# Kernel tuning notes

Measured on AMD Instinct MI355X. Metric: run time of the kernel, lower is better.

Reference implementation:

```python
import jax, jax.numpy as jnp
import numpy as np

NUM_GRAPHS = 64

def _mlp(x, Wa, ba, Wb, bb):
    # 2-layer MLP: Linear -> ReLU -> Linear
    return jnp.maximum(x @ Wa + ba, 0.0) @ Wb + bb

def setup_inputs() -> dict:
    key = jax.random.key(0)
    ks = jax.random.split(key, 16)
    N1, E1, N2, E2 = 20000, 640000, 640000, 1280000
    d_x1, d_x2, d_e2, d_h, d_et, d_out = 32, 32, 16, 64, 32, 32
    inp = {
        'x1': jax.random.normal(ks[0], (N1, d_x1), jnp.float32),
        'x2': jax.random.normal(ks[1], (N2, d_x2), jnp.float32),
        'edge_index1': jax.random.randint(ks[2], (2, E1), 0, N1),
        'edge_index2': jax.random.randint(ks[3], (2, E2), 0, N2),
        'x1_batch': jnp.sort(jax.random.randint(ks[4], (N1,), 0, NUM_GRAPHS)),
        'edge_attr2': jax.random.normal(ks[5], (E2, d_e2), jnp.float32),
        # mlp2 (DGCN edge network): in = d_x2 + d_e2 = 48 -> 64 -> 32
        'W2a': jax.random.normal(ks[6], (d_x2 + d_e2, d_h), jnp.float32) * 0.05,
        'b2a': jnp.zeros((d_h,), jnp.float32),
        'W2b': jax.random.normal(ks[7], (d_h, d_et), jnp.float32) * 0.05,
        'b2b': jnp.zeros((d_et,), jnp.float32),
        # mlp (MOLGCN edge-conditioned network): in = d_x1 + d_et = 64 -> 64 -> 32
        'W1a': jax.random.normal(ks[8], (d_x1 + d_et, d_h), jnp.float32) * 0.05,
        'b1a': jnp.zeros((d_h,), jnp.float32),
        'W1b': jax.random.normal(ks[9], (d_h, d_out), jnp.float32) * 0.05,
        'b1b': jnp.zeros((d_out,), jnp.float32),
    }
    return inp

def reference(x1, x2, edge_index1, edge_index2, x1_batch, edge_attr2,
              W2a, b2a, W2b, b2b, W1a, b1a, W1b, b1b):
    N1, N2 = x1.shape[0], x2.shape[0]
    # --- DGCN over graph 2: message = mlp2([x_src, edge_attr]), sum-aggregate at dst ---
    s2, d2 = edge_index2[0], edge_index2[1]
    msg2 = _mlp(jnp.concatenate([x2[s2], edge_attr2], axis=-1), W2a, b2a, W2b, b2b)  # [E2, d_et]
    e_t = jax.ops.segment_sum(msg2, d2, num_segments=N2)  # [N2, d_et]; N2 == E1 (line graph)
    # --- MOLGCN over graph 1: edge-conditioned message = mlp([x_src, e_t]), sum at dst ---
    s1, d1 = edge_index1[0], edge_index1[1]
    msg1 = _mlp(jnp.concatenate([x1[s1], e_t], axis=-1), W1a, b1a, W1b, b1b)  # [E1, d_out]
    h = jax.ops.segment_sum(msg1, d1, num_segments=N1)  # [N1, d_out]
    # --- global add pool over graphs, then squeeze()/2 ---
    pooled = jax.ops.segment_sum(h, x1_batch, num_segments=NUM_GRAPHS)  # [G, d_out]
    return jnp.squeeze(pooled) / 2.0
```

## Files before the change

kernel.cpp:

```cpp
#include <hip/hip_runtime.h>
#include <hip/hip_bf16.h>


#define NUM_GRAPHS 64
#define CAP 4608
#define CURSTRIDE 16
#define EPB 8192
#define NCVT 2048

typedef __attribute__((ext_vector_type(8))) short bf16x8;
typedef __attribute__((ext_vector_type(4))) float f32x4;

__device__ __forceinline__ unsigned short f2bf(float x) {
    __hip_bfloat16 b = __float2bfloat16(x);
    return *(unsigned short*)&b;
}
__device__ __forceinline__ float bf2f(unsigned int u16) {
    unsigned short us = (unsigned short)u16;
    __hip_bfloat16 b = *(__hip_bfloat16*)&us;
    return __bfloat162float(b);
}
__device__ __forceinline__ unsigned int pack2(float lo, float hi) {
    return (unsigned int)f2bf(lo) | ((unsigned int)f2bf(hi) << 16);
}
__device__ __forceinline__ uint4 cvt8(const float* src) {
    const float4* s4 = (const float4*)src;
    float4 a = s4[0], b = s4[1];
    return make_uint4(pack2(a.x, a.y), pack2(a.z, a.w),
                      pack2(b.x, b.y), pack2(b.z, b.w));
}
__device__ __forceinline__ int swz(int row, int kb) {
    return row * 128 + (kb ^ ((row & 7) << 4));
}


__global__ __launch_bounds__(256) void k_prep0(
    const float* __restrict__ W2a, const float* __restrict__ b2a,
    const float* __restrict__ W2b, const float* __restrict__ b2b,
    const float* __restrict__ W1a, const float* __restrict__ b1a,
    const float* __restrict__ W1b, const float* __restrict__ b1b,
    unsigned char* __restrict__ wpack, int* __restrict__ cur, int ncur)
{
    const int tid = threadIdx.x;
    if (blockIdx.x == 0) {
        unsigned char* img1 = wpack;
        unsigned char* img2 = wpack + 12672;
        for (int i = tid; i < 64 * 64; i += 256) {
            int n = i >> 6, k = i & 63;
            float v1 = (k < 48) ? W2a[k * 64 + n] : 0.0f;
            *(unsigned short*)(img1 + n * 128 + ((2 * k) ^ ((n & 7) << 4))) = f2bf(v1);
            *(unsigned short*)(img2 + n * 128 + ((2 * k) ^ ((n & 7) << 4))) = f2bf(W1a[k * 64 + n]);
        }
        for (int i = tid; i < 32 * 64; i += 256) {
            int n = i >> 6, k = i & 63;
            *(unsigned short*)(img1 + 8192 + n * 128 + ((2 * k) ^ ((n & 7) << 4))) = f2bf(W2b[k * 32 + n]);
            *(unsigned short*)(img2 + 8192 + n * 128 + ((2 * k) ^ ((n & 7) << 4))) = f2bf(W1b[k * 32 + n]);
        }
        if (tid < 64) {
            ((float*)(img1 + 12288))[tid] = b2a[tid];
            ((float*)(img2 + 12288))[tid] = b1a[tid];
        }
        if (tid < 32) {
            ((float*)(img1 + 12544))[tid] = b2b[tid];
            ((float*)(img2 + 12544))[tid] = b1b[tid];
        }
    } else {
        for (int i = tid; i < ncur; i += 256) cur[i] = 0;
    }
}


__global__ __launch_bounds__(256) void k_bscat_cvt(
    const int* __restrict__ ei2, int E2, const int* __restrict__ ei1, int E1,
    int* __restrict__ cur, uint2* __restrict__ mid, int NB2, int NBT, int Etot, int NBB,
    const float* __restrict__ x2, uint4* __restrict__ x2b,
    const float* __restrict__ x1, uint4* __restrict__ x1b,
    const float* __restrict__ ea2, uint4* __restrict__ ea2b,
    long xn2, long xn1, long xne)
{
    __shared__ unsigned int buck[EPB];
    __shared__ int hist[512];
    __shared__ int gbase[512];
    __shared__ int wloc[512];

    const int tid = threadIdx.x;
    if (blockIdx.x >= NBB) {
        const long tot = xn2 + xn1 + xne;
        const long stride = (long)NCVT * 256;
        for (long i = (long)(blockIdx.x - NBB) * 256 + tid; i < tot; i += stride) {
            if (i < xn2) x2b[i] = cvt8(x2 + i * 8);
            else if (i < xn2 + xn1) { long j = i - xn2; x1b[j] = cvt8(x1 + j * 8); }
            else { long j = i - xn2 - xn1; ea2b[j] = cvt8(ea2 + j * 8); }
        }
        return;
    }

    const long start = (long)blockIdx.x * EPB;
    const int nloc = (int)(((long)Etot - start) < EPB ? ((long)Etot - start) : EPB);
    if (nloc <= 0) return;

    for (int i = tid; i < NBT; i += 256) hist[i] = 0;
    __syncthreads();

    for (int k = tid; k < nloc; k += 256) {
        const long i = start + k;
        int b, dlo;
        if (i < E2) {
            int d = ei2[E2 + i]; b = d >> 11; dlo = d & 2047;
        } else {
            int j = (int)(i - E2);
            int d = ei1[E1 + j]; b = NB2 + (d >> 7); dlo = d & 127;
        }
        buck[k] = (unsigned)b | ((unsigned)dlo << 16);
        atomicAdd(&hist[b], 1);
    }
    __syncthreads();

    for (int i = tid; i < NBT; i += 256) {
        const int c = hist[i];
        gbase[i] = (c > 0) ? atomicAdd(&cur[i * CURSTRIDE], c) : 0;
        wloc[i] = 0;
    }
    __syncthreads();

    for (int k = tid; k < nloc; k += 256) {
        const long i = start + k;
        const unsigned bv = buck[k];
        const int b = (int)(bv & 0xffffu), dlo = (int)(bv >> 16);
        int e, s;
        if (i < E2) { e = (int)i; s = ei2[i]; }
        else        { int j = (int)(i - E2); e = j; s = ei1[j]; }
        const int pos = gbase[b] + atomicAdd(&wloc[b], 1);
        if (pos < CAP)
            mid[(size_t)b * CAP + pos] =
                make_uint2((unsigned)e | ((unsigned)dlo << 21), (unsigned)s);
    }
}


__global__ __launch_bounds__(256) void k_csr(
    const int* __restrict__ cur, const uint2* __restrict__ mid,
    uint2* __restrict__ ord, int NB2, int E2)
{
    __shared__ int cnt[2048];
    __shared__ int cnt2[2048];
    __shared__ int red[256];
    __shared__ int wpart[4];
    __shared__ int sCarry;

    const int b = blockIdx.x, tid = threadIdx.x;
    const bool g2 = (b < NB2);
    const int span = g2 ? 2048 : 128;
    const int lo = g2 ? 0 : NB2;
    const int fill = min(cur[b * CURSTRIDE], CAP);

    int part = 0;
    for (int k = lo + tid; k < b; k += 256) part += min(cur[k * CURSTRIDE], CAP);
    red[tid] = part;
    __syncthreads();
    for (int off = 128; off >= 1; off >>= 1) {
        if (tid < off) red[tid] += red[tid + off];
        __syncthreads();
    }
    const int outBase = (g2 ? 0 : E2) + red[0];

    for (int k = tid; k < span; k += 256) cnt[k] = 0;
    __syncthreads();

    const size_t mbase = (size_t)b * CAP;
    for (int i = tid; i < fill; i += 256)
        atomicAdd(&cnt[mid[mbase + i].x >> 21], 1);
    __syncthreads();

    if (tid == 0) sCarry = 0;
    __syncthreads();
    const int lane = tid & 63, wv = tid >> 6;
    for (int c0 = 0; c0 < span; c0 += 256) {
        const int idx = c0 + tid;
        int v = (idx < span) ? cnt[idx] : 0;
        int inc = v;
        #pragma unroll
        for (int off = 1; off < 64; off <<= 1) {
            int nv = __shfl_up(inc, off, 64);
            if (lane >= off) inc += nv;
        }
        if (lane == 63) wpart[wv] = inc;
        __syncthreads();
        int wpre = 0;
        for (int wq = 0; wq < wv; ++wq) wpre += wpart[wq];
        const int excl = sCarry + wpre + inc - v;
        const int tot = wpart[0] + wpart[1] + wpart[2] + wpart[3];
        __syncthreads();
        if (idx < span) cnt[idx] = excl;
        if (tid == 0) sCarry += tot;
        __syncthreads();
    }

    for (int k = tid; k < span; k += 256) cnt2[k] = 0;
    __syncthreads();

    for (int i = tid; i < fill; i += 256) {
        uint2 r = mid[mbase + i];
        const int dl = (int)(r.x >> 21);
        const int rk = atomicAdd(&cnt2[dl], 1);
        ord[outBase + cnt[dl] + rk] = make_uint2(r.x, r.y | ((unsigned)b << 20));
    }
}


__global__ __launch_bounds__(256) void k_msg2_agg(
    const float* __restrict__ x2f, const uint4* __restrict__ x2b,
    const float* __restrict__ ea2, const uint4* __restrict__ ea2b,
    const uint2* __restrict__ ord, const unsigned char* __restrict__ wimg,
    unsigned int* __restrict__ e_t, int E, int use_bf16, int use_ea2b)
{
    __shared__ __align__(16) unsigned char sBuf[32768];
    unsigned short* smsg = (unsigned short*)sBuf;
    int* sdst = (int*)(sBuf + 16896);
    int* rstart = (int*)(sBuf + 16896 + 1032);
    unsigned long long* wmaskS = (unsigned long long*)(sBuf + 16896 + 1032 + 1032);

    const int tid = threadIdx.x;
    const int base = blockIdx.x * 256, p = base + tid;

    int e = 0, s = 0, d = -1, dp_ = -1, dn_ = -1;
    if (p < E) {
        uint2 o = ord[p];
        e = (int)(o.x & 0x1FFFFFu); s = (int)(o.y & 0xFFFFFu);
        d = ((int)(o.y >> 20) << 11) + (int)(o.x >> 21);
    }
    if (tid == 0) {
        if (base > 0) { uint2 o = ord[base - 1]; dp_ = ((int)(o.y >> 20) << 11) + (int)(o.x >> 21); }
        if (base + 256 < E) { uint2 o = ord[base + 256]; dn_ = ((int)(o.y >> 20) << 11) + (int)(o.x >> 21); }
    }

    {
        uint4 ch[8];
        if (use_bf16) {
            const uint4* xr = x2b + (size_t)s * 4;
            #pragma unroll
            for (int c = 0; c < 4; ++c) ch[c] = xr[c];
        } else {
            const float4* xs = (const float4*)(x2f + (size_t)s * 32);
            #pragma unroll
            for (int c = 0; c < 4; ++c) {
                float4 a = xs[2 * c], b = xs[2 * c + 1];
                ch[c].x = pack2(a.x, a.y); ch[c].y = pack2(a.z, a.w);
                ch[c].z = pack2(b.x, b.y); ch[c].w = pack2(b.z, b.w);
            }
        }
        if (use_ea2b) {
            ch[4] = ea2b[(size_t)e * 2];
            ch[5] = ea2b[(size_t)e * 2 + 1];
        } else {
            const float4* es = (const float4*)(ea2 + (size_t)e * 16);
            #pragma unroll
            for (int c = 0; c < 2; ++c) {
                float4 a = es[2 * c], b = es[2 * c + 1];
                ch[4 + c].x = pack2(a.x, a.y); ch[4 + c].y = pack2(a.z, a.w);
                ch[4 + c].z = pack2(b.x, b.y); ch[4 + c].w = pack2(b.z, b.w);
            }
        }
        ch[6] = make_uint4(0, 0, 0, 0);
        ch[7] = make_uint4(0, 0, 0, 0);
        #pragma unroll
        for (int c = 0; c < 8; ++c)
            *(uint4*)(sBuf + swz(tid, c * 16)) = ch[c];
    }
    __syncthreads();

    const int lane = tid & 63, wv = tid >> 6;
    const int lr = lane & 15, lk = lane >> 4;
    const int band = wv * 64;
    const unsigned char* gWa = wimg;
    const unsigned char* gWb = wimg + 8192;
    const float* gba = (const float*)(wimg + 12288);
    const float* gbb = (const float*)(wimg + 12544);

    f32x4 accA[4][4];
    #pragma unroll
    for (int n = 0; n < 4; ++n) {
        float bv = gba[n * 16 + lr];
        #pragma unroll
        for (int m = 0; m < 4; ++m) accA[m][n] = (f32x4){bv, bv, bv, bv};
    }
    #pragma unroll
    for (int ks = 0; ks < 2; ++ks) {
        const int kb = ks * 64 + lk * 16;
        bf16x8 af[4], bfr[4];
        #pragma unroll
        for (int m = 0; m < 4; ++m)
            af[m] = *(const bf16x8*)(sBuf + swz(band + m * 16 + lr, kb));
        #pragma unroll
        for (int n = 0; n < 4; ++n) {
            int rw = n * 16 + lr;
            bfr[n] = *(const bf16x8*)(gWa + rw * 128 + (kb ^ ((rw & 7) << 4)));
        }
        #pragma unroll
        for (int m = 0; m < 4; ++m)
            #pragma unroll
            for (int n = 0; n < 4; ++n)
                accA[m][n] = __builtin_amdgcn_mfma_f32_16x16x32_bf16(af[m], bfr[n], accA[m][n], 0, 0, 0);
    }
    #pragma unroll
    for (int m = 0; m < 4; ++m)
        #pragma unroll
        for (int n = 0; n < 4; ++n)
            #pragma unroll
            for (int rr = 0; rr < 4; ++rr) {
                int grow = band + m * 16 + lk * 4 + rr;
                int cb = 2 * (n * 16 + lr);
                *(unsigned short*)(sBuf + swz(grow, cb)) = f2bf(fmaxf(accA[m][n][rr], 0.0f));
            }

    f32x4 accB[4][2];
    #pragma unroll
    for (int n = 0; n < 2; ++n) {
        float bv = gbb[n * 16 + lr];
        #pragma unroll
        for (int m = 0; m < 4; ++m) accB[m][n] = (f32x4){bv, bv, bv, bv};
    }
    #pragma unroll
    for (int ks = 0; ks < 2; ++ks) {
        const int kb = ks * 64 + lk * 16;
        bf16x8 af[4], bfr[2];
        #pragma unroll
        for (int m = 0; m < 4; ++m)
            af[m] = *(const bf16x8*)(sBuf + swz(band + m * 16 + lr, kb));
        #pragma unroll
        for (int n = 0; n < 2; ++n) {
            int rw = n * 16 + lr;
            bfr[n] = *(const bf16x8*)(gWb + rw * 128 + (kb ^ ((rw & 7) << 4)));
        }
        #pragma unroll
        for (int m = 0; m < 4; ++m)
            #pragma unroll
            for (int n = 0; n < 2; ++n)
                accB[m][n] = __builtin_amdgcn_mfma_f32_16x16x32_bf16(af[m], bfr[n], accB[m][n], 0, 0, 0);
    }
    __syncthreads();

    #pragma unroll
    for (int m = 0; m < 4; ++m)
        #pragma unroll
        for (int n = 0; n < 2; ++n)
            #pragma unroll
            for (int rr = 0; rr < 4; ++rr)
                smsg[(band + m * 16 + lk * 4 + rr) * 33 + n * 16 + lr] = f2bf(accB[m][n][rr]);
    sdst[tid] = d;
    if (tid == 0) { sdst[256] = dn_; sdst[257] = dp_; }
    __syncthreads();

    const bool leader = (p < E) && (tid == 0 || sdst[tid - 1] != d);
    wmaskS[wv] = __ballot(leader);
    __syncthreads();

    int nruns = __popcll(wmaskS[0]) + __popcll(wmaskS[1]) + __popcll(wmaskS[2]) + __popcll(wmaskS[3]);
    if (leader) {
        int before = __popcll(wmaskS[wv] & ((1ULL << lane) - 1));
        for (int w = 0; w < wv; ++w) before += __popcll(wmaskS[w]);
        rstart[before] = tid;
    }
    const int vcnt = (E - base < 256) ? (E - base) : 256;
    if (tid == 0) rstart[nruns] = vcnt;
    __syncthreads();

    const int sPrev = sdst[257];
    const int ntask = nruns * 32;
    for (int task = tid; task < ntask; task += 256) {
        const int run = task >> 5, c = task & 31;
        const int rs = rstart[run], re = rstart[run + 1];
        const int dd = sdst[rs];
        float acc = 0.0f;
        for (int qq = rs; qq < re; ++qq) acc += bf2f(smsg[qq * 33 + c]);
        const bool gs = (rs > 0) || (base == 0) || (sPrev != dd);
        const bool ge = (re < 256) || (sdst[256] != dd);
        if (gs && ge) {
            ((unsigned short*)e_t)[(size_t)dd * 32 + c] = f2bf(acc);
        } else {
            unsigned int* a32 = e_t + (size_t)dd * 16 + (c >> 1);
            const int sh = (c & 1) * 16;
            unsigned int old = *a32;
            while (true) {
                float cur2 = bf2f((old >> sh) & 0xffffu);
                unsigned int nb = f2bf(cur2 + acc);
                unsigned int nv = (old & ~(0xffffu << sh)) | (nb << sh);
                unsigned int prev = atomicCAS(a32, old, nv);
                if (prev == old) break;
                old = prev;
            }
        }
    }
}


__global__ __launch_bounds__(256) void k_msg1_agg(
    const float* __restrict__ x1f, const uint4* __restrict__ x1b,
    const unsigned int* __restrict__ e_t,
    const uint2* __restrict__ ord, const unsigned char* __restrict__ wimg,
    float* __restrict__ h, int E, int NB2, int use_bf16)
{
    __shared__ __align__(16) unsigned char sBuf[32768];
    unsigned short* smsg = (unsigned short*)sBuf;
    int* sdst = (int*)(sBuf + 16896);
    int* rstart = (int*)(sBuf + 16896 + 1032);
    unsigned long long* wmaskS = (unsigned long long*)(sBuf + 16896 + 1032 + 1032);

    const int tid = threadIdx.x;
    const int base = blockIdx.x * 256, p = base + tid;

    int e = 0, s = 0, d = -1, dp_ = -1, dn_ = -1;
    if (p < E) {
        uint2 o = ord[p];
        e = (int)(o.x & 0x1FFFFFu); s = (int)(o.y & 0xFFFFFu);
        d = (((int)(o.y >> 20) - NB2) << 7) + (int)(o.x >> 21);
    }
    if (tid == 0) {
        if (base > 0) { uint2 o = ord[base - 1]; dp_ = (((int)(o.y >> 20) - NB2) << 7) + (int)(o.x >> 21); }
        if (base + 256 < E) { uint2 o = ord[base + 256]; dn_ = (((int)(o.y >> 20) - NB2) << 7) + (int)(o.x >> 21); }
    }

    {
        uint4 ch[8];
        if (use_bf16) {
            const uint4* xr = x1b + (size_t)s * 4;
            #pragma unroll
            for (int c = 0; c < 4; ++c) ch[c] = xr[c];
        } else {
            const float4* xs = (const float4*)(x1f + (size_t)s * 32);
            #pragma unroll
            for (int c = 0; c < 4; ++c) {
                float4 a = xs[2 * c], b = xs[2 * c + 1];
                ch[c].x = pack2(a.x, a.y); ch[c].y = pack2(a.z, a.w);
                ch[c].z = pack2(b.x, b.y); ch[c].w = pack2(b.z, b.w);
            }
        }
        const uint4* er = (const uint4*)(e_t + (size_t)e * 16);
        #pragma unroll
        for (int c = 0; c < 4; ++c) ch[4 + c] = er[c];
        #pragma unroll
        for (int c = 0; c < 8; ++c)
            *(uint4*)(sBuf + swz(tid, c * 16)) = ch[c];
    }
    __syncthreads();

    const int lane = tid & 63, wv = tid >> 6;
    const int lr = lane & 15, lk = lane >> 4;
    const int band = wv * 64;
    const unsigned char* gWa = wimg;
    const unsigned char* gWb = wimg + 8192;
    const float* gba = (const float*)(wimg + 12288);
    const float* gbb = (const float*)(wimg + 12544);

    f32x4 accA[4][4];
    #pragma unroll
    for (int n = 0; n < 4; ++n) {
        float bv = gba[n * 16 + lr];
        #pragma unroll
        for (int m = 0; m < 4; ++m) accA[m][n] = (f32x4){bv, bv, bv, bv};
    }
    #pragma unroll
    for (int ks = 0; ks < 2; ++ks) {
        const int kb = ks * 64 + lk * 16;
        bf16x8 af[4], bfr[4];
        #pragma unroll
        for (int m = 0; m < 4; ++m)
            af[m] = *(const bf16x8*)(sBuf + swz(band + m * 16 + lr, kb));
        #pragma unroll
        for (int n = 0; n < 4; ++n) {
            int rw = n * 16 + lr;
            bfr[n] = *(const bf16x8*)(gWa + rw * 128 + (kb ^ ((rw & 7) << 4)));
        }
        #pragma unroll
        for (int m = 0; m < 4; ++m)
            #pragma unroll
            for (int n = 0; n < 4; ++n)
                accA[m][n] = __builtin_amdgcn_mfma_f32_16x16x32_bf16(af[m], bfr[n], accA[m][n], 0, 0, 0);
    }
    #pragma unroll
    for (int m = 0; m < 4; ++m)
        #pragma unroll
        for (int n = 0; n < 4; ++n)
            #pragma unroll
            for (int rr = 0; rr < 4; ++rr) {
                int grow = band + m * 16 + lk * 4 + rr;
                int cb = 2 * (n * 16 + lr);
                *(unsigned short*)(sBuf + swz(grow, cb)) = f2bf(fmaxf(accA[m][n][rr], 0.0f));
            }

    f32x4 accB[4][2];
    #pragma unroll
    for (int n = 0; n < 2; ++n) {
        float bv = gbb[n * 16 + lr];
        #pragma unroll
        for (int m = 0; m < 4; ++m) accB[m][n] = (f32x4){bv, bv, bv, bv};
    }
    #pragma unroll
    for (int ks = 0; ks < 2; ++ks) {
        const int kb = ks * 64 + lk * 16;
        bf16x8 af[4], bfr[2];
        #pragma unroll
        for (int m = 0; m < 4; ++m)
            af[m] = *(const bf16x8*)(sBuf + swz(band + m * 16 + lr, kb));
        #pragma unroll
        for (int n = 0; n < 2; ++n) {
            int rw = n * 16 + lr;
            bfr[n] = *(const bf16x8*)(gWb + rw * 128 + (kb ^ ((rw & 7) << 4)));
        }
        #pragma unroll
        for (int m = 0; m < 4; ++m)
            #pragma unroll
            for (int n = 0; n < 2; ++n)
                accB[m][n] = __builtin_amdgcn_mfma_f32_16x16x32_bf16(af[m], bfr[n], accB[m][n], 0, 0, 0);
    }
    __syncthreads();

    #pragma unroll
    for (int m = 0; m < 4; ++m)
        #pragma unroll
        for (int n = 0; n < 2; ++n)
            #pragma unroll
            for (int rr = 0; rr < 4; ++rr)
                smsg[(band + m * 16 + lk * 4 + rr) * 33 + n * 16 + lr] = f2bf(accB[m][n][rr]);
    sdst[tid] = d;
    if (tid == 0) { sdst[256] = dn_; sdst[257] = dp_; }
    __syncthreads();

    const bool leader = (p < E) && (tid == 0 || sdst[tid - 1] != d);
    wmaskS[wv] = __ballot(leader);
    __syncthreads();

    int nruns = __popcll(wmaskS[0]) + __popcll(wmaskS[1]) + __popcll(wmaskS[2]) + __popcll(wmaskS[3]);
    if (leader) {
        int before = __popcll(wmaskS[wv] & ((1ULL << lane) - 1));
        for (int w = 0; w < wv; ++w) before += __popcll(wmaskS[w]);
        rstart[before] = tid;
    }
    const int vcnt = (E - base < 256) ? (E - base) : 256;
    if (tid == 0) rstart[nruns] = vcnt;
    __syncthreads();

    const int sPrev = sdst[257];
    const int ntask = nruns * 32;
    for (int task = tid; task < ntask; task += 256) {
        const int run = task >> 5, c = task & 31;
        const int rs = rstart[run], re = rstart[run + 1];
        const int dd = sdst[rs];
        float acc = 0.0f;
        for (int qq = rs; qq < re; ++qq) acc += bf2f(smsg[qq * 33 + c]);
        const bool gs = (rs > 0) || (base == 0) || (sPrev != dd);
        const bool ge = (re < 256) || (sdst[256] != dd);
        if (gs && ge) h[(size_t)dd * 32 + c] = acc;
        else atomicAdd(h + (size_t)dd * 32 + c, acc);
    }
}


__device__ __forceinline__ int lower_bound_i(const int* a, int n, int key) {
    int lo = 0, hi = n;
    while (lo < hi) {
        int mid = (lo + hi) >> 1;
        if (a[mid] < key) lo = mid + 1; else hi = mid;
    }
    return lo;
}

__global__ __launch_bounds__(256) void k_pool(const float* __restrict__ h,
                                              const int* __restrict__ batch,
                                              float* __restrict__ out, int N1) {
    const int g = blockIdx.x;
    const int lo = lower_bound_i(batch, N1, g);
    const int hi = lower_bound_i(batch, N1, g + 1);
    const int tid = threadIdx.x;
    const int c = tid & 31, rg = tid >> 5;
    float acc = 0.0f;
    for (int n = lo + rg; n < hi; n += 8) acc += h[(size_t)n * 32 + c];
    __shared__ float red[256];
    red[tid] = acc;
    __syncthreads();
    for (int off = 128; off >= 32; off >>= 1) {
        if (tid < off) red[tid] += red[tid + off];
        __syncthreads();
    }
    if (tid < 32) out[g * 32 + tid] = red[tid] * 0.5f;
}


extern "C" void kernel_launch(void* const* d_in, const int* in_sizes, int n_in,
                              void* d_out, int out_size, void* d_ws, size_t ws_size,
                              hipStream_t stream) {
    const float* x1  = (const float*)d_in[0];
    const float* x2  = (const float*)d_in[1];
    const int*   ei1 = (const int*)d_in[2];
    const int*   ei2 = (const int*)d_in[3];
    const int*   xb  = (const int*)d_in[4];
    const float* ea2 = (const float*)d_in[5];
    const float* W2a = (const float*)d_in[6];
    const float* b2a = (const float*)d_in[7];
    const float* W2b = (const float*)d_in[8];
    const float* b2b = (const float*)d_in[9];
    const float* W1a = (const float*)d_in[10];
    const float* b1a = (const float*)d_in[11];
    const float* W1b = (const float*)d_in[12];
    const float* b1b = (const float*)d_in[13];

    const int N1 = in_sizes[0] / 32;
    const int E1 = in_sizes[2] / 2;
    const int E2 = in_sizes[3] / 2;
    const int N2 = in_sizes[1] / 32;
    const int Etot = E2 + E1;

    const int NB2 = (N2 + 2047) >> 11;
    const int NB1 = (N1 + 127) >> 7;
    const int NBT = NB2 + NB1;

    const size_t sz_wpack = 25600;
    const size_t sz_cur   = (size_t)NBT * CURSTRIDE * 4;
    const size_t sz_et    = (size_t)N2 * 64;
    const size_t sz_h     = (size_t)N1 * 128;
    const size_t sz_ord   = (size_t)Etot * 8;
    const size_t sz_mid   = (size_t)NBT * CAP * 8;
    const size_t regA     = (sz_mid > sz_et + sz_h) ? sz_mid : (sz_et + sz_h);
    const size_t sz_x2b   = (size_t)N2 * 64;
    const size_t sz_x1b   = (size_t)N1 * 64;
    const size_t sz_ea2b  = (size_t)E2 * 32;
    const size_t need_x   = sz_ord + regA + sz_x2b + sz_x1b + sz_wpack + sz_cur;
    const size_t need_xe  = need_x + sz_ea2b;

    const int use_bf16 = (ws_size >= need_x) ? 1 : 0;
    const int use_ea2b = (ws_size >= need_xe) ? 1 : 0;

    char* w = (char*)d_ws;
    uint2* ord = (uint2*)w;            w += sz_ord;
    char* regionA = w;                 w += regA;
    uint4* x2b = (uint4*)w;            if (use_bf16) w += sz_x2b;
    uint4* x1b = (uint4*)w;            if (use_bf16) w += sz_x1b;
    uint4* ea2b = (uint4*)w;           if (use_ea2b) w += sz_ea2b;
    unsigned char* wpack = (unsigned char*)w;  w += sz_wpack;
    int* cur = (int*)w;

    unsigned int* e_t = (unsigned int*)regionA;
    float* h = (float*)(regionA + sz_et);
    uint2* mid = (uint2*)regionA;

    const int NBB = (Etot + EPB - 1) / EPB;
    const long xn2 = use_bf16 ? (long)N2 * 4 : 0;
    const long xn1 = use_bf16 ? (long)N1 * 4 : 0;
    const long xne = use_ea2b ? (long)E2 * 2 : 0;

    k_prep0<<<2, 256, 0, stream>>>(W2a, b2a, W2b, b2b, W1a, b1a, W1b, b1b,
                                   wpack, cur, NBT * CURSTRIDE);
    k_bscat_cvt<<<NBB + NCVT, 256, 0, stream>>>(
        ei2, E2, ei1, E1, cur, mid, NB2, NBT, Etot, NBB,
        x2, x2b, x1, x1b, ea2, ea2b, xn2, xn1, xne);
    k_csr<<<NBT, 256, 0, stream>>>(cur, mid, ord, NB2, E2);
    hipMemsetAsync(regionA, 0, sz_et + sz_h, stream);
    k_msg2_agg<<<(E2 + 255) / 256, 256, 0, stream>>>(
        x2, x2b, ea2, ea2b, ord, wpack, e_t, E2, use_bf16, use_ea2b);
    k_msg1_agg<<<(E1 + 255) / 256, 256, 0, stream>>>(
        x1, x1b, e_t, ord + E2, wpack + 12672, h, E1, NB2, use_bf16);
    k_pool<<<NUM_GRAPHS, 256, 0, stream>>>(h, xb, (float*)d_out, N1);
}
```

Baseline: 262.1 us.

## Store e_t rows in graph-1 CSR order so msg1 reads them contiguously

Splits the CSR build into two kernels. The graph-1 pass runs first and records the sorted rank of each line-graph node. The graph-2 pass then relabels its destinations with that rank, so msg2 aggregation writes e_t rows in the order msg1 consumes them. msg1 then reads e_t sequentially by its own position instead of gathering by edge id, which replaces a random 64-byte-row gather with coalesced loads. In exchange it adds an extra kernel launch, a rank array, and a random rank lookup in the graph-2 CSR pass, and graph-2 destinations may now be less clustered, which could hurt its segmented reduction.

```diff
diff --git a/kernel.cpp b/kernel.cpp
--- a/kernel.cpp
+++ b/kernel.cpp
@@ -138,40 +138,9 @@
 }
 
 
-__global__ __launch_bounds__(256) void k_csr(
-    const int* __restrict__ cur, const uint2* __restrict__ mid,
-    uint2* __restrict__ ord, int NB2, int E2)
-{
-    __shared__ int cnt[2048];
-    __shared__ int cnt2[2048];
-    __shared__ int red[256];
+__device__ __forceinline__ void lds_excl_scan(int* cnt, int span, int tid) {
     __shared__ int wpart[4];
     __shared__ int sCarry;
-
-    const int b = blockIdx.x, tid = threadIdx.x;
-    const bool g2 = (b < NB2);
-    const int span = g2 ? 2048 : 128;
-    const int lo = g2 ? 0 : NB2;
-    const int fill = min(cur[b * CURSTRIDE], CAP);
-
-    int part = 0;
-    for (int k = lo + tid; k < b; k += 256) part += min(cur[k * CURSTRIDE], CAP);
-    red[tid] = part;
-    __syncthreads();
-    for (int off = 128; off >= 1; off >>= 1) {
-        if (tid < off) red[tid] += red[tid + off];
-        __syncthreads();
-    }
-    const int outBase = (g2 ? 0 : E2) + red[0];
-
-    for (int k = tid; k < span; k += 256) cnt[k] = 0;
-    __syncthreads();
-
-    const size_t mbase = (size_t)b * CAP;
-    for (int i = tid; i < fill; i += 256)
-        atomicAdd(&cnt[mid[mbase + i].x >> 21], 1);
-    __syncthreads();
-
     if (tid == 0) sCarry = 0;
     __syncthreads();
     const int lane = tid & 63, wv = tid >> 6;
@@ -195,15 +164,90 @@
         if (tid == 0) sCarry += tot;
         __syncthreads();
     }
-
-    for (int k = tid; k < span; k += 256) cnt2[k] = 0;
-    __syncthreads();
-
+}
+
+
+__global__ __launch_bounds__(256) void k_csr1(
+    const int* __restrict__ cur, const uint2* __restrict__ mid,
+    uint2* __restrict__ ord1, int* __restrict__ rank1, int NB2)
+{
+    __shared__ int cnt[128];
+    __shared__ int cnt2[128];
+    __shared__ int red[256];
+
+    const int bl = blockIdx.x, tid = threadIdx.x;
+    const int bg = NB2 + bl;
+    const int fill = min(cur[bg * CURSTRIDE], CAP);
+
+    int part = 0;
+    for (int k = NB2 + tid; k < bg; k += 256) part += min(cur[k * CURSTRIDE], CAP);
+    red[tid] = part;
+    __syncthreads();
+    for (int off = 128; off >= 1; off >>= 1) {
+        if (tid < off) red[tid] += red[tid + off];
+        __syncthreads();
+    }
+    const int outBase = red[0];
+
+    if (tid < 128) { cnt[tid] = 0; cnt2[tid] = 0; }
+    __syncthreads();
+    const size_t mbase = (size_t)bg * CAP;
+    for (int i = tid; i < fill; i += 256)
+        atomicAdd(&cnt[mid[mbase + i].x >> 21], 1);
+    __syncthreads();
+    lds_excl_scan(cnt, 128, tid);
+    __syncthreads();
     for (int i = tid; i < fill; i += 256) {
         uint2 r = mid[mbase + i];
         const int dl = (int)(r.x >> 21);
         const int rk = atomicAdd(&cnt2[dl], 1);
-        ord[outBase + cnt[dl] + rk] = make_uint2(r.x, r.y | ((unsigned)b << 20));
+        const int o = outBase + cnt[dl] + rk;
+        ord1[o] = make_uint2(r.x, r.y | ((unsigned)bg << 20));
+        rank1[r.x & 0x1FFFFFu] = o;
+    }
+}
+
+
+__global__ __launch_bounds__(256) void k_csr2(
+    const int* __restrict__ cur, const uint2* __restrict__ mid,
+    uint2* __restrict__ ord2, const int* __restrict__ rank1, int E1)
+{
+    __shared__ int cnt[2048];
+    __shared__ int cnt2[2048];
+    __shared__ int red[256];
+
+    const int b = blockIdx.x, tid = threadIdx.x;
+    const int node0 = b << 11;
+    const int fill = min(cur[b * CURSTRIDE], CAP);
+
+    int part = 0;
+    for (int k = tid; k < b; k += 256) part += min(cur[k * CURSTRIDE], CAP);
+    red[tid] = part;
+    __syncthreads();
+    for (int off = 128; off >= 1; off >>= 1) {
+        if (tid < off) red[tid] += red[tid + off];
+        __syncthreads();
+    }
+    const int outBase = red[0];
+
+    for (int k = tid; k < 2048; k += 256) { cnt[k] = 0; cnt2[k] = 0; }
+    __syncthreads();
+    const size_t mbase = (size_t)b * CAP;
+    for (int i = tid; i < fill; i += 256)
+        atomicAdd(&cnt[mid[mbase + i].x >> 21], 1);
+    __syncthreads();
+    lds_excl_scan(cnt, 2048, tid);
+    __syncthreads();
+    for (int i = tid; i < fill; i += 256) {
+        uint2 r = mid[mbase + i];
+        const int dl = (int)(r.x >> 21);
+        const int e  = (int)(r.x & 0x1FFFFFu);
+        const int rk = atomicAdd(&cnt2[dl], 1);
+        const int o = outBase + cnt[dl] + rk;
+        unsigned key = (unsigned)rank1[node0 + dl];
+        if (key >= (unsigned)E1) key = 0;
+        ord2[o] = make_uint2((unsigned)e | ((key & 0x7FFu) << 21),
+                             r.y | ((key >> 11) << 20));
     }
 }
 
@@ -227,11 +271,11 @@
     if (p < E) {
         uint2 o = ord[p];
         e = (int)(o.x & 0x1FFFFFu); s = (int)(o.y & 0xFFFFFu);
-        d = ((int)(o.y >> 20) << 11) + (int)(o.x >> 21);
+        d = (int)((o.x >> 21) | ((o.y >> 20) << 11));
     }
     if (tid == 0) {
-        if (base > 0) { uint2 o = ord[base - 1]; dp_ = ((int)(o.y >> 20) << 11) + (int)(o.x >> 21); }
-        if (base + 256 < E) { uint2 o = ord[base + 256]; dn_ = ((int)(o.y >> 20) << 11) + (int)(o.x >> 21); }
+        if (base > 0) { uint2 o = ord[base - 1]; dp_ = (int)((o.x >> 21) | ((o.y >> 20) << 11)); }
+        if (base + 256 < E) { uint2 o = ord[base + 256]; dn_ = (int)((o.x >> 21) | ((o.y >> 20) << 11)); }
     }
 
     {
@@ -409,10 +453,10 @@
     const int tid = threadIdx.x;
     const int base = blockIdx.x * 256, p = base + tid;
 
-    int e = 0, s = 0, d = -1, dp_ = -1, dn_ = -1;
+    int s = 0, d = -1, dp_ = -1, dn_ = -1;
     if (p < E) {
         uint2 o = ord[p];
-        e = (int)(o.x & 0x1FFFFFu); s = (int)(o.y & 0xFFFFFu);
+        s = (int)(o.y & 0xFFFFFu);
         d = (((int)(o.y >> 20) - NB2) << 7) + (int)(o.x >> 21);
     }
     if (tid == 0) {
@@ -435,7 +479,8 @@
                 ch[c].z = pack2(b.x, b.y); ch[c].w = pack2(b.z, b.w);
             }
         }
-        const uint4* er = (const uint4*)(e_t + (size_t)e * 16);
+        const int erow = (p < E) ? p : (E - 1);
+        const uint4* er = (const uint4*)(e_t + (size_t)erow * 16);
         #pragma unroll
         for (int c = 0; c < 4; ++c) ch[4 + c] = er[c];
         #pragma unroll
@@ -620,7 +665,9 @@
     const size_t sz_h     = (size_t)N1 * 128;
     const size_t sz_ord   = (size_t)Etot * 8;
     const size_t sz_mid   = (size_t)NBT * CAP * 8;
-    const size_t regA     = (sz_mid > sz_et + sz_h) ? sz_mid : (sz_et + sz_h);
+    const size_t sz_rank  = (size_t)N2 * 4;
+    const size_t regA     = ((sz_mid + sz_rank) > sz_et + sz_h) ? (sz_mid + sz_rank)
+                                                                : (sz_et + sz_h);
     const size_t sz_x2b   = (size_t)N2 * 64;
     const size_t sz_x1b   = (size_t)N1 * 64;
     const size_t sz_ea2b  = (size_t)E2 * 32;
@@ -642,6 +689,7 @@
     unsigned int* e_t = (unsigned int*)regionA;
     float* h = (float*)(regionA + sz_et);
     uint2* mid = (uint2*)regionA;
+    int* rank1 = (int*)(regionA + sz_mid);
 
     const int NBB = (Etot + EPB - 1) / EPB;
     const long xn2 = use_bf16 ? (long)N2 * 4 : 0;
@@ -653,7 +701,8 @@
     k_bscat_cvt<<<NBB + NCVT, 256, 0, stream>>>(
         ei2, E2, ei1, E1, cur, mid, NB2, NBT, Etot, NBB,
         x2, x2b, x1, x1b, ea2, ea2b, xn2, xn1, xne);
-    k_csr<<<NBT, 256, 0, stream>>>(cur, mid, ord, NB2, E2);
+    k_csr1<<<NB1, 256, 0, stream>>>(cur, mid, ord + E2, rank1, NB2);
+    k_csr2<<<NB2, 256, 0, stream>>>(cur, mid, ord, rank1, E1);
     hipMemsetAsync(regionA, 0, sz_et + sz_h, stream);
     k_msg2_agg<<<(E2 + 255) / 256, 256, 0, stream>>>(
         x2, x2b, ea2, ea2b, ord, wpack, e_t, E2, use_bf16, use_ea2b);
```

New measurement: 278.4 us. 1.06x slower.
